# Optimization experiments

Measured on AMD Instinct MI355X. Metric: run time of the kernel, lower is better.

Reference implementation:

```python
import math
import jax, jax.numpy as jnp
import numpy as np

B, S, D, H = 2, 2048, 1024, 16
DH = D // H


def setup_inputs() -> dict:
    key = jax.random.key(0)
    ks = jax.random.split(key, 12)
    s = 1.0 / math.sqrt(D)
    return {
        "x_q": jax.random.normal(ks[0], (B, S, D), jnp.float32),
        "x_k": jax.random.normal(ks[1], (B, S, D), jnp.float32),
        "x_v": jax.random.normal(ks[2], (B, S, D), jnp.float32),
        "mask": jax.random.randint(ks[3], (B, S), 0, 2) > 0,
        "Wq": jax.random.normal(ks[4], (D, D), jnp.float32) * s,
        "bq": jnp.zeros((D,), jnp.float32),
        "Wk": jax.random.normal(ks[5], (D, D), jnp.float32) * s,
        "bk": jnp.zeros((D,), jnp.float32),
        "Wv": jax.random.normal(ks[6], (D, D), jnp.float32) * s,
        "bv": jnp.zeros((D,), jnp.float32),
        "Wo": jax.random.normal(ks[7], (D, D), jnp.float32) * s,
        "bo": jnp.zeros((D,), jnp.float32),
    }


def reference(x_q, x_k, x_v, mask, Wq, bq, Wk, bk, Wv, bv, Wo, bo):
    # nn.Linear: y = x @ W^T + b
    Q = jnp.einsum('bsd,ed->bse', x_q, Wq) + bq
    K = jnp.einsum('bsd,ed->bse', x_k, Wk) + bk
    V = jnp.einsum('bsd,ed->bse', x_v, Wv) + bv
    b, sq, d = Q.shape
    # split(dim_split, 2) + cat(dim=0) == per-head attention on [B,S,H,DH]
    Qh = Q.reshape(b, sq, H, DH)
    Kh = K.reshape(b, -1, H, DH)
    Vh = V.reshape(b, -1, H, DH)
    scores = jnp.einsum('bqhd,bkhd->bhqk', Qh, Kh) / math.sqrt(DH)
    # inf_mask: -1e9 where mask is False, broadcast over heads and queries
    scores = scores + jnp.where(mask[:, None, None, :], 0.0, -1e9)
    A = jax.nn.softmax(scores, axis=-1)  # dropout is identity in eval
    out = jnp.einsum('bhqk,bkhd->bqhd', A, Vh).reshape(b, sq, d)
    return jnp.einsum('bsd,ed->bse', out, Wo) + bo
```

## Files before the change

kernel.cpp:

```cpp
#include <hip/hip_runtime.h>
#include <hip/hip_bf16.h>
#include <stdint.h>

#define BB  2
#define SS  2048
#define DDIM 1024
#define HH  16
#define DH  64

typedef __attribute__((ext_vector_type(8))) short short8;
typedef __attribute__((ext_vector_type(4))) short short4v;
typedef __attribute__((ext_vector_type(4))) float float4v;
typedef __attribute__((ext_vector_type(2))) unsigned int uint2v;

#define AS1 __attribute__((address_space(1)))
#define AS3 __attribute__((address_space(3)))

static __device__ __forceinline__ void gl2lds16(const void* g, void* l) {
  __builtin_amdgcn_global_load_lds((const AS1 unsigned int*)g,
                                   (AS3 unsigned int*)l, 16, 0, 0);
}

static __device__ __forceinline__ float bf2f(short s) {
  union { unsigned u; float f; } c;
  c.u = ((unsigned)(unsigned short)s) << 16;
  return c.f;
}
static __device__ __forceinline__ short f2bf(float f) {
  union { float ff; unsigned u; } c;
  c.ff = f;
  unsigned u = c.u;
  u += 0x7fffu + ((u >> 16) & 1u);
  return (short)(u >> 16);
}

#if __has_builtin(__builtin_amdgcn_exp2f)
static __device__ __forceinline__ float exp2fast(float x) { return __builtin_amdgcn_exp2f(x); }
#else
static __device__ __forceinline__ float exp2fast(float x) { return __expf(x * 0.69314718056f); }
#endif

static __device__ __forceinline__ unsigned packbf(float x, float y) {
  unsigned ax = __float_as_uint(x) + 0x8000u;
  unsigned ay = __float_as_uint(y) + 0x8000u;
#if __has_builtin(__builtin_amdgcn_perm)
  return __builtin_amdgcn_perm(ay, ax, 0x07060302u);
#else
  return (ax >> 16) | (ay & 0xffff0000u);
#endif
}

static __device__ __forceinline__ int detect_f32(const void* p) {
  const float* f = (const float*)p;
  int ok = 1;
#pragma unroll
  for (int i = 0; i < 16; i++) {
    float a = fabsf(f[i]);
    ok &= (a > 1e-10f && a < 1e4f) ? 1 : 0;
  }
  return ok;
}

struct CvtArgs {
  const void* xq; const void* xk; const void* xv;
  const void* wq; const void* wk; const void* wv; const void* wo;
  const void* b0; const void* b1; const void* b2; const void* b3;
  short* dst;
};

__global__ __launch_bounds__(256)
void cvt_kernel(CvtArgs a) {
  const int f32m = detect_f32(a.xq);
  const size_t gtid = (size_t)blockIdx.x * blockDim.x + threadIdx.x;
  const size_t stride = (size_t)gridDim.x * blockDim.x;
  const size_t M4 = (size_t)4 << 20, M1 = (size_t)1 << 20, TOT = (size_t)16 << 20;
  for (size_t i = gtid; i * 4 < TOT; i += stride) {
    const size_t idx = i * 4;
    const void* src;
    size_t off;
    if (idx < 3 * M4) {
      size_t xi = idx / M4;
      off = idx & (M4 - 1);
      src = (xi == 0) ? a.xq : (xi == 1) ? a.xk : a.xv;
    } else {
      size_t wi = (idx - 3 * M4) / M1;
      off = idx & (M1 - 1);
      src = (wi == 0) ? a.wq : (wi == 1) ? a.wk : (wi == 2) ? a.wv : a.wo;
    }
    short4v o;
    if (f32m) {
      float4v v = *(const float4v*)((const float*)src + off);
#pragma unroll
      for (int j = 0; j < 4; j++) o[j] = f2bf(v[j]);
    } else {
      o = *(const short4v*)((const short*)src + off);
    }
    *(short4v*)(a.dst + idx) = o;
  }
  if (gtid < 1024) {
    const void* bs[4] = {a.b0, a.b1, a.b2, a.b3};
#pragma unroll
    for (int j = 0; j < 4; j++) {
      short v = f32m ? f2bf(((const float*)bs[j])[gtid])
                     : ((const short*)bs[j])[gtid];
      a.dst[TOT + (size_t)j * 1024 + gtid] = v;
    }
  }
}

struct GemmArgs {
  const short* x[3];
  const short* w[3];
  const short* b[3];
  short* o[3];
  const void* probe;
  int tmask;
  int detect_out;
};

__global__ __launch_bounds__(256)
void gemm_kernel(GemmArgs a) {
  constexpr int GK = 1024, GN = 1024;
  __shared__ alignas(16) short As[128 * 32];
  __shared__ alignas(16) short Bs[128 * 32];

  const int t = threadIdx.x;
  const int w = t >> 6, l = t & 63, l15 = l & 15, qd = l >> 4;
  const int bn = blockIdx.x, bm = blockIdx.y, mat = blockIdx.z;

  const short* X  = a.x[mat];
  const short* W  = a.w[mat];
  const short* Bi = a.b[mat];
  short* O        = a.o[mat];
  const int transposed = (a.tmask >> mat) & 1;

  const short* Ag = X + (size_t)bm * 128 * GK;
  const short* Bg = W + (size_t)bn * 128 * GK;

  const int L0 = t, L1 = 256 + t;
  const int r0 = L0 >> 2, g0 = (L0 & 3) ^ ((r0 >> 1) & 3);
  const int r1 = L1 >> 2, g1 = (L1 & 3) ^ ((r1 >> 1) & 3);
  const size_t off0 = (size_t)r0 * GK + g0 * 8;
  const size_t off1 = (size_t)r1 * GK + g1 * 8;

  float4v acc[4][4];
#pragma unroll
  for (int i = 0; i < 4; i++)
#pragma unroll
    for (int j = 0; j < 4; j++) acc[i][j] = (float4v){0.f, 0.f, 0.f, 0.f};

  const int wm = (w >> 1) * 64, wn = (w & 1) * 64;

  for (int k0 = 0; k0 < GK; k0 += 32) {
    gl2lds16(Ag + off0 + k0, (char*)As + L0 * 16);
    gl2lds16(Ag + off1 + k0, (char*)As + L1 * 16);
    gl2lds16(Bg + off0 + k0, (char*)Bs + L0 * 16);
    gl2lds16(Bg + off1 + k0, (char*)Bs + L1 * 16);
    __syncthreads();

    short8 af[4], bf[4];
#pragma unroll
    for (int i = 0; i < 4; i++) {
      int m = wm + i * 16 + l15;
      af[i] = *(const short8*)((const char*)As + (m * 4 + (qd ^ ((m >> 1) & 3))) * 16);
      int n = wn + i * 16 + l15;
      bf[i] = *(const short8*)((const char*)Bs + (n * 4 + (qd ^ ((n >> 1) & 3))) * 16);
    }
#pragma unroll
    for (int i = 0; i < 4; i++)
#pragma unroll
      for (int j = 0; j < 4; j++)
        acc[i][j] = __builtin_amdgcn_mfma_f32_16x16x32_bf16(af[i], bf[j], acc[i][j], 0, 0, 0);
    __syncthreads();
  }

  if (!transposed) {
    const int outf32 = a.detect_out ? detect_f32(a.probe) : 0;
    float bj[4];
#pragma unroll
    for (int j = 0; j < 4; j++) bj[j] = bf2f(Bi[bn * 128 + wn + j * 16 + l15]);
#pragma unroll
    for (int i = 0; i < 4; i++) {
      int mgl = bm * 128 + wm + i * 16 + qd * 4;
#pragma unroll
      for (int j = 0; j < 4; j++) {
        int ngl = bn * 128 + wn + j * 16 + l15;
        if (outf32) {
          float* Of = (float*)O;
#pragma unroll
          for (int r = 0; r < 4; r++)
            Of[(size_t)(mgl + r) * GN + ngl] = acc[i][j][r] + bj[j];
        } else {
#pragma unroll
          for (int r = 0; r < 4; r++)
            O[(size_t)(mgl + r) * GN + ngl] = f2bf(acc[i][j][r] + bj[j]);
        }
      }
    }
  } else {
#pragma unroll
    for (int j = 0; j < 4; j++) {
      int ngl = bn * 128 + wn + j * 16 + l15;
      float bb = bf2f(Bi[ngl]);
#pragma unroll
      for (int i = 0; i < 4; i++) {
        int mgl = bm * 128 + wm + i * 16 + qd * 4;
        int bidx = mgl >> 11;
        int s = mgl & (SS - 1);
        short4v v;
#pragma unroll
        for (int r = 0; r < 4; r++) v[r] = f2bf(acc[i][j][r] + bb);
        *(short4v*)(O + (size_t)bidx * DDIM * SS + (size_t)ngl * SS + s) = v;
      }
    }
  }
}

__global__ __launch_bounds__(256)
void flash_kernel(const short* __restrict__ Q, const short* __restrict__ K,
                  const short* __restrict__ Vt, const int* __restrict__ mask,
                  short* __restrict__ Oa) {
  __shared__ alignas(16) short Ks[2][32 * 64];
  __shared__ alignas(16) short Vs[2][64 * 32];
  __shared__ alignas(16) float madd[2][32];
  __shared__ alignas(16) short Ps[4][2][16 * 40];

  const int t = threadIdx.x;
  const int w = t >> 6, l = t & 63, l15 = l & 15, qd = l >> 4;
  const int qt = blockIdx.x, bh = blockIdx.y;
  const int b = bh >> 4, h = bh & 15;
  const int q0 = qt * 128 + w * 32;

  const float SC = 0.125f * 1.44269504f;
  const float MC = 16.0f * 1.44269504f;

  short8 qf[2][2];
#pragma unroll
  for (int g = 0; g < 2; g++) {
    const short* Qb = Q + ((size_t)(b * SS + q0 + 16 * g + l15)) * DDIM + h * 64;
#pragma unroll
    for (int c = 0; c < 2; c++) qf[g][c] = *(const short8*)(Qb + 32 * c + 8 * qd);
  }

  const int kr = t >> 3;
  const short* Kg = K + ((size_t)(b * SS + kr)) * DDIM + h * 64 + (((t & 7) ^ (kr & 7)) * 8);
  const int vr = t >> 2;
  const short* Vg = Vt + (size_t)b * DDIM * SS + (size_t)(h * 64 + vr) * SS
                    + (((t & 3) ^ ((vr >> 1) & 3)) * 8);
  const int* Mg = mask + b * SS;

  const int sw = l15 & 7;
  int kOff[2], vOff[4];
#pragma unroll
  for (int mt = 0; mt < 2; mt++) kOff[mt] = (mt * 16 + l15) * 64 + ((qd ^ sw) * 8);
  const int vchunk = qd ^ ((l15 >> 1) & 3);
#pragma unroll
  for (int mt = 0; mt < 4; mt++) vOff[mt] = (mt * 16 + l15) * 32 + vchunk * 8;

  float4v oacc[2][4];
#pragma unroll
  for (int g = 0; g < 2; g++)
#pragma unroll
    for (int mt = 0; mt < 4; mt++) oacc[g][mt] = (float4v){0.f, 0.f, 0.f, 0.f};
  float lsum[2] = {0.f, 0.f};

  gl2lds16(Kg, (char*)Ks[0] + t * 16);
  gl2lds16(Vg, (char*)Vs[0] + t * 16);
  int mv = 0;
  if (t < 32) {
    mv = Mg[t];
    madd[0][t] = mv ? -MC : -1e9f;
    mv = Mg[32 + t];
  }

  for (int i = 0; i < SS / 32; i++) {
    const int cur = i & 1, nxt = cur ^ 1;
    asm volatile("s_waitcnt vmcnt(0) lgkmcnt(0)\n\ts_barrier" ::: "memory");

    if (i < SS / 32 - 1) {
      gl2lds16(Kg + (size_t)(i + 1) * 32 * DDIM, (char*)Ks[nxt] + t * 16);
      gl2lds16(Vg + (i + 1) * 32, (char*)Vs[nxt] + t * 16);
    }
    if (t < 32) {
      madd[nxt][t] = mv ? -MC : -1e9f;
      int idx = 32 * i + 64 + t;
      if (idx > SS - 1) idx = SS - 1;
      mv = Mg[idx];
    }

    const short* ksb = Ks[cur];
    const short* vsb = Vs[cur];

    float4v sacc[2][2];
#pragma unroll
    for (int g = 0; g < 2; g++)
#pragma unroll
      for (int mt = 0; mt < 2; mt++) sacc[g][mt] = (float4v){0.f, 0.f, 0.f, 0.f};
#pragma unroll
    for (int mt = 0; mt < 2; mt++) {
      short8 kf0 = *(const short8*)(ksb + kOff[mt]);
      short8 kf1 = *(const short8*)(ksb + (kOff[mt] ^ 32));
#pragma unroll
      for (int g = 0; g < 2; g++) {
        sacc[g][mt] = __builtin_amdgcn_mfma_f32_16x16x32_bf16(kf0, qf[g][0], sacc[g][mt], 0, 0, 0);
        sacc[g][mt] = __builtin_amdgcn_mfma_f32_16x16x32_bf16(kf1, qf[g][1], sacc[g][mt], 0, 0, 0);
      }
    }

    float4v ma[2];
#pragma unroll
    for (int mt = 0; mt < 2; mt++)
      ma[mt] = *(const float4v*)(&madd[cur][16 * mt + 4 * qd]);

    short8 vf[4];
#pragma unroll
    for (int mt = 0; mt < 4; mt++) vf[mt] = *(const short8*)(vsb + vOff[mt]);

#pragma unroll
    for (int g = 0; g < 2; g++) {
      float p[2][4];
#pragma unroll
      for (int mt = 0; mt < 2; mt++)
#pragma unroll
        for (int r = 0; r < 4; r++) {
          p[mt][r] = exp2fast(fmaf(sacc[g][mt][r], SC, ma[mt][r]));
          lsum[g] += p[mt][r];
        }
      short* pw = (short*)Ps[w][g] + l15 * 40;
#pragma unroll
      for (int mt = 0; mt < 2; mt++) {
        uint2v pk;
        pk[0] = packbf(p[mt][0], p[mt][1]);
        pk[1] = packbf(p[mt][2], p[mt][3]);
        *(uint2v*)(pw + mt * 16 + qd * 4) = pk;
      }
      asm volatile("s_waitcnt lgkmcnt(0)" ::: "memory");
      short8 pf = *(const short8*)((short*)Ps[w][g] + l15 * 40 + qd * 8);

#pragma unroll
      for (int mt = 0; mt < 4; mt++)
        oacc[g][mt] = __builtin_amdgcn_mfma_f32_16x16x32_bf16(vf[mt], pf, oacc[g][mt], 0, 0, 0);
    }
  }

#pragma unroll
  for (int g = 0; g < 2; g++) {
    lsum[g] += __shfl_xor(lsum[g], 16);
    lsum[g] += __shfl_xor(lsum[g], 32);
    const float inv = 1.f / lsum[g];
    short* Og = Oa + ((size_t)(b * SS + q0 + 16 * g + l15)) * DDIM + h * 64;
#pragma unroll
    for (int mt = 0; mt < 4; mt++) {
      short4v v;
#pragma unroll
      for (int r = 0; r < 4; r++) v[r] = f2bf(oacc[g][mt][r] * inv);
      *(short4v*)(Og + mt * 16 + qd * 4) = v;
    }
  }
}

extern "C" void kernel_launch(void* const* d_in, const int* in_sizes, int n_in,
                              void* d_out, int out_size, void* d_ws, size_t ws_size,
                              hipStream_t stream) {
  (void)in_sizes; (void)n_in; (void)out_size; (void)ws_size;
  const int* mask = (const int*)d_in[3];

  char* ws = (char*)d_ws;
  short* wsBF = (short*)ws;
  const size_t M1 = (size_t)1 << 20;
  short* Qb = (short*)(ws + (size_t)34 * M1);
  short* Kb = (short*)(ws + (size_t)42 * M1);
  short* Vt = (short*)(ws + (size_t)50 * M1);
  short* At = (short*)(ws + (size_t)58 * M1);

  CvtArgs c;
  c.xq = d_in[0]; c.xk = d_in[1]; c.xv = d_in[2];
  c.wq = d_in[4]; c.wk = d_in[6]; c.wv = d_in[8]; c.wo = d_in[10];
  c.b0 = d_in[5]; c.b1 = d_in[7]; c.b2 = d_in[9]; c.b3 = d_in[11];
  c.dst = wsBF;
  hipLaunchKernelGGL(cvt_kernel, dim3(4096), dim3(256), 0, stream, c);

  GemmArgs a1;
  a1.x[0] = wsBF;            a1.x[1] = wsBF + 4 * M1;  a1.x[2] = wsBF + 8 * M1;
  a1.w[0] = wsBF + 12 * M1;  a1.w[1] = wsBF + 13 * M1; a1.w[2] = wsBF + 14 * M1;
  a1.b[0] = wsBF + 16 * M1;  a1.b[1] = wsBF + 16 * M1 + 1024;
  a1.b[2] = wsBF + 16 * M1 + 2048;
  a1.o[0] = Qb; a1.o[1] = Kb; a1.o[2] = Vt;
  a1.probe = d_in[0];
  a1.tmask = 4;
  a1.detect_out = 0;
  hipLaunchKernelGGL(gemm_kernel, dim3(8, 32, 3), dim3(256), 0, stream, a1);

  hipLaunchKernelGGL(flash_kernel, dim3(16, 32), dim3(256), 0, stream,
                     Qb, Kb, Vt, mask, At);

  GemmArgs a2;
  a2.x[0] = At;             a2.w[0] = wsBF + 15 * M1;
  a2.b[0] = wsBF + 16 * M1 + 3072;
  a2.o[0] = (short*)d_out;
  a2.x[1] = a2.x[2] = At; a2.w[1] = a2.w[2] = a2.w[0];
  a2.b[1] = a2.b[2] = a2.b[0]; a2.o[1] = a2.o[2] = a2.o[0];
  a2.probe = d_in[0];
  a2.tmask = 0;
  a2.detect_out = 1;
  hipLaunchKernelGGL(gemm_kernel, dim3(8, 32, 1), dim3(256), 0, stream, a2);
}
```

Measured before the change: 258.7 us.

## Split flash attention over the key dimension and add a combine kernel

The flash kernel grid gains a key-split dimension (two halves when workspace permits). Each split writes fp32 partial outputs and row sums, and a new combine kernel adds them, normalizes and writes bf16. The row sum is now computed by an extra MFMA against a ones vector instead of scalar adds and shuffles. This doubles the flash grid from 512 blocks to improve occupancy on the many CUs, at the cost of extra fp32 partial traffic (about 32MB written and read) and one more launch.

```diff
diff --git a/kernel.cpp b/kernel.cpp
--- a/kernel.cpp
+++ b/kernel.cpp
@@ -219,7 +219,8 @@
 __global__ __launch_bounds__(256)
 void flash_kernel(const short* __restrict__ Q, const short* __restrict__ K,
                   const short* __restrict__ Vt, const int* __restrict__ mask,
-                  short* __restrict__ Oa) {
+                  short* __restrict__ At, float* __restrict__ Op,
+                  float* __restrict__ Lw, int nsplit) {
   __shared__ alignas(16) short Ks[2][32 * 64];
   __shared__ alignas(16) short Vs[2][64 * 32];
   __shared__ alignas(16) float madd[2][32];
@@ -227,9 +228,11 @@
 
   const int t = threadIdx.x;
   const int w = t >> 6, l = t & 63, l15 = l & 15, qd = l >> 4;
-  const int qt = blockIdx.x, bh = blockIdx.y;
+  const int qt = blockIdx.x, bh = blockIdx.y, split = blockIdx.z;
   const int b = bh >> 4, h = bh & 15;
   const int q0 = qt * 128 + w * 32;
+  const int kspan = SS / nsplit;
+  const int kbase = split * kspan;
 
   const float SC = 0.125f * 1.44269504f;
   const float MC = 16.0f * 1.44269504f;
@@ -242,12 +245,17 @@
     for (int c = 0; c < 2; c++) qf[g][c] = *(const short8*)(Qb + 32 * c + 8 * qd);
   }
 
+  const short onebf = (short)0x3F80;
+  const short ov = (l15 == 0) ? onebf : (short)0;
+  const short8 onesf = {ov, ov, ov, ov, ov, ov, ov, ov};
+
   const int kr = t >> 3;
-  const short* Kg = K + ((size_t)(b * SS + kr)) * DDIM + h * 64 + (((t & 7) ^ (kr & 7)) * 8);
+  const short* Kg = K + ((size_t)(b * SS + kbase + kr)) * DDIM + h * 64
+                    + (((t & 7) ^ (kr & 7)) * 8);
   const int vr = t >> 2;
   const short* Vg = Vt + (size_t)b * DDIM * SS + (size_t)(h * 64 + vr) * SS
-                    + (((t & 3) ^ ((vr >> 1) & 3)) * 8);
-  const int* Mg = mask + b * SS;
+                    + kbase + (((t & 3) ^ ((vr >> 1) & 3)) * 8);
+  const int* Mg = mask + b * SS + kbase;
 
   const int sw = l15 & 7;
   int kOff[2], vOff[4];
@@ -258,11 +266,13 @@
   for (int mt = 0; mt < 4; mt++) vOff[mt] = (mt * 16 + l15) * 32 + vchunk * 8;
 
   float4v oacc[2][4];
-#pragma unroll
-  for (int g = 0; g < 2; g++)
+  float4v oaccl[2];
+#pragma unroll
+  for (int g = 0; g < 2; g++) {
+    oaccl[g] = (float4v){0.f, 0.f, 0.f, 0.f};
 #pragma unroll
     for (int mt = 0; mt < 4; mt++) oacc[g][mt] = (float4v){0.f, 0.f, 0.f, 0.f};
-  float lsum[2] = {0.f, 0.f};
+  }
 
   gl2lds16(Kg, (char*)Ks[0] + t * 16);
   gl2lds16(Vg, (char*)Vs[0] + t * 16);
@@ -273,18 +283,19 @@
     mv = Mg[32 + t];
   }
 
-  for (int i = 0; i < SS / 32; i++) {
+  const int niter = kspan / 32;
+  for (int i = 0; i < niter; i++) {
     const int cur = i & 1, nxt = cur ^ 1;
     asm volatile("s_waitcnt vmcnt(0) lgkmcnt(0)\n\ts_barrier" ::: "memory");
 
-    if (i < SS / 32 - 1) {
+    if (i < niter - 1) {
       gl2lds16(Kg + (size_t)(i + 1) * 32 * DDIM, (char*)Ks[nxt] + t * 16);
       gl2lds16(Vg + (i + 1) * 32, (char*)Vs[nxt] + t * 16);
     }
     if (t < 32) {
       madd[nxt][t] = mv ? -MC : -1e9f;
       int idx = 32 * i + 64 + t;
-      if (idx > SS - 1) idx = SS - 1;
+      if (idx > kspan - 1) idx = kspan - 1;
       mv = Mg[idx];
     }
 
@@ -322,10 +333,8 @@
 #pragma unroll
       for (int mt = 0; mt < 2; mt++)
 #pragma unroll
-        for (int r = 0; r < 4; r++) {
+        for (int r = 0; r < 4; r++)
           p[mt][r] = exp2fast(fmaf(sacc[g][mt][r], SC, ma[mt][r]));
-          lsum[g] += p[mt][r];
-        }
       short* pw = (short*)Ps[w][g] + l15 * 40;
 #pragma unroll
       for (int mt = 0; mt < 2; mt++) {
@@ -340,29 +349,61 @@
 #pragma unroll
       for (int mt = 0; mt < 4; mt++)
         oacc[g][mt] = __builtin_amdgcn_mfma_f32_16x16x32_bf16(vf[mt], pf, oacc[g][mt], 0, 0, 0);
-    }
-  }
-
-#pragma unroll
-  for (int g = 0; g < 2; g++) {
-    lsum[g] += __shfl_xor(lsum[g], 16);
-    lsum[g] += __shfl_xor(lsum[g], 32);
-    const float inv = 1.f / lsum[g];
-    short* Og = Oa + ((size_t)(b * SS + q0 + 16 * g + l15)) * DDIM + h * 64;
-#pragma unroll
-    for (int mt = 0; mt < 4; mt++) {
-      short4v v;
-#pragma unroll
-      for (int r = 0; r < 4; r++) v[r] = f2bf(oacc[g][mt][r] * inv);
-      *(short4v*)(Og + mt * 16 + qd * 4) = v;
-    }
-  }
+      oaccl[g] = __builtin_amdgcn_mfma_f32_16x16x32_bf16(onesf, pf, oaccl[g], 0, 0, 0);
+    }
+  }
+
+  if (nsplit == 2) {
+    float* OpS = Op + (size_t)split * ((size_t)4 << 20);
+#pragma unroll
+    for (int g = 0; g < 2; g++) {
+      const int q = q0 + 16 * g + l15;
+      float* base = OpS + ((size_t)(b * SS + q)) * DDIM + h * 64;
+#pragma unroll
+      for (int mt = 0; mt < 4; mt++)
+        *(float4v*)(base + mt * 16 + qd * 4) = oacc[g][mt];
+      if (qd == 0)
+        Lw[split * (BB * HH * SS) + (b * HH + h) * SS + q] = oaccl[g][0];
+    }
+  } else {
+#pragma unroll
+    for (int g = 0; g < 2; g++) {
+      const float lg = __shfl(oaccl[g][0], l15);
+      const float inv = 1.f / lg;
+      short* Og = At + ((size_t)(b * SS + q0 + 16 * g + l15)) * DDIM + h * 64;
+#pragma unroll
+      for (int mt = 0; mt < 4; mt++) {
+        short4v v;
+#pragma unroll
+        for (int r = 0; r < 4; r++) v[r] = f2bf(oacc[g][mt][r] * inv);
+        *(short4v*)(Og + mt * 16 + qd * 4) = v;
+      }
+    }
+  }
+}
+
+__global__ __launch_bounds__(256)
+void combine_kernel(const float* __restrict__ Op, const float* __restrict__ Lw,
+                    short* __restrict__ At) {
+  const int tid = blockIdx.x * 256 + threadIdx.x;
+  const size_t e4 = (size_t)tid * 4;
+  const int row = (int)(e4 >> 10);
+  const int col = (int)(e4 & 1023);
+  const int b = row >> 11, q = row & (SS - 1), h = col >> 6;
+  float4v o0 = *(const float4v*)(Op + e4);
+  float4v o1 = *(const float4v*)(Op + ((size_t)4 << 20) + e4);
+  const int li = (b * HH + h) * SS + q;
+  const float inv = 1.f / (Lw[li] + Lw[BB * HH * SS + li]);
+  short4v v;
+#pragma unroll
+  for (int r = 0; r < 4; r++) v[r] = f2bf((o0[r] + o1[r]) * inv);
+  *(short4v*)(At + e4) = v;
 }
 
 extern "C" void kernel_launch(void* const* d_in, const int* in_sizes, int n_in,
                               void* d_out, int out_size, void* d_ws, size_t ws_size,
                               hipStream_t stream) {
-  (void)in_sizes; (void)n_in; (void)out_size; (void)ws_size;
+  (void)in_sizes; (void)n_in; (void)out_size;
   const int* mask = (const int*)d_in[3];
 
   char* ws = (char*)d_ws;
@@ -372,6 +413,10 @@
   short* Kb = (short*)(ws + (size_t)42 * M1);
   short* Vt = (short*)(ws + (size_t)50 * M1);
   short* At = (short*)(ws + (size_t)58 * M1);
+  float* Op = (float*)(ws + (size_t)66 * M1);
+  float* Lw = (float*)(ws + (size_t)98 * M1);
+
+  const int nsplit = (ws_size >= (size_t)99 * M1) ? 2 : 1;
 
   CvtArgs c;
   c.xq = d_in[0]; c.xk = d_in[1]; c.xv = d_in[2];
@@ -391,8 +436,12 @@
   a1.detect_out = 0;
   hipLaunchKernelGGL(gemm_kernel, dim3(8, 32, 3), dim3(256), 0, stream, a1);
 
-  hipLaunchKernelGGL(flash_kernel, dim3(16, 32), dim3(256), 0, stream,
-                     Qb, Kb, Vt, mask, At);
+  hipLaunchKernelGGL(flash_kernel, dim3(16, 32, nsplit), dim3(256), 0, stream,
+                     Qb, Kb, Vt, mask, At, Op, Lw, nsplit);
+
+  if (nsplit == 2)
+    hipLaunchKernelGGL(combine_kernel, dim3(4096), dim3(256), 0, stream,
+                       Op, Lw, At);
 
   GemmArgs a2;
   a2.x[0] = At;             a2.w[0] = wsBF + 15 * M1;
```

New measurement: 272.5 us. 1.05x slower.

## Make flash attention warp-private with per-warp KV staging, MFMA row sums, precomputed mask

Applied to the files above, without the earlier changes.

Restructures the flash kernel so each 64-lane wave loads its own K/V tiles into private LDS double buffers, which removes block-wide barriers. Blocks shrink to 128 threads and the grid is reordered. P is packed straight into MFMA operand registers instead of round-tripping through LDS. Row sums are computed with an extra MFMA against a ones vector, and the mask additive term is precomputed once in the convert kernel into a float workspace. The cost is duplicated K/V loads per wave, more global traffic, and an extra MFMA per step.

```diff
diff --git a/kernel.cpp b/kernel.cpp
--- a/kernel.cpp
+++ b/kernel.cpp
@@ -11,7 +11,6 @@
 typedef __attribute__((ext_vector_type(8))) short short8;
 typedef __attribute__((ext_vector_type(4))) short short4v;
 typedef __attribute__((ext_vector_type(4))) float float4v;
-typedef __attribute__((ext_vector_type(2))) unsigned int uint2v;
 
 #define AS1 __attribute__((address_space(1)))
 #define AS3 __attribute__((address_space(3)))
@@ -65,7 +64,9 @@
   const void* xq; const void* xk; const void* xv;
   const void* wq; const void* wk; const void* wv; const void* wo;
   const void* b0; const void* b1; const void* b2; const void* b3;
+  const int* mask;
   short* dst;
+  float* mw;
 };
 
 __global__ __launch_bounds__(256)
@@ -106,6 +107,8 @@
       a.dst[TOT + (size_t)j * 1024 + gtid] = v;
     }
   }
+  if (gtid < BB * SS)
+    a.mw[gtid] = a.mask[gtid] ? -23.083120654223414f : -1e9f;
 }
 
 struct GemmArgs {
@@ -216,23 +219,20 @@
   }
 }
 
-__global__ __launch_bounds__(256)
+__global__ __launch_bounds__(128)
 void flash_kernel(const short* __restrict__ Q, const short* __restrict__ K,
-                  const short* __restrict__ Vt, const int* __restrict__ mask,
-                  short* __restrict__ Oa) {
-  __shared__ alignas(16) short Ks[2][32 * 64];
-  __shared__ alignas(16) short Vs[2][64 * 32];
-  __shared__ alignas(16) float madd[2][32];
-  __shared__ alignas(16) short Ps[4][2][16 * 40];
+                  const short* __restrict__ Vt, const float* __restrict__ Mw,
+                  short* __restrict__ At) {
+  __shared__ alignas(16) short Kbuf[2][2][2048];
+  __shared__ alignas(16) short Vbuf[2][2][2048];
 
   const int t = threadIdx.x;
   const int w = t >> 6, l = t & 63, l15 = l & 15, qd = l >> 4;
-  const int qt = blockIdx.x, bh = blockIdx.y;
+  const int bh = blockIdx.x, qt = blockIdx.y;
   const int b = bh >> 4, h = bh & 15;
-  const int q0 = qt * 128 + w * 32;
+  const int q0 = qt * 64 + w * 32;
 
   const float SC = 0.125f * 1.44269504f;
-  const float MC = 16.0f * 1.44269504f;
 
   short8 qf[2][2];
 #pragma unroll
@@ -242,54 +242,63 @@
     for (int c = 0; c < 2; c++) qf[g][c] = *(const short8*)(Qb + 32 * c + 8 * qd);
   }
 
-  const int kr = t >> 3;
-  const short* Kg = K + ((size_t)(b * SS + kr)) * DDIM + h * 64 + (((t & 7) ^ (kr & 7)) * 8);
-  const int vr = t >> 2;
-  const short* Vg = Vt + (size_t)b * DDIM * SS + (size_t)(h * 64 + vr) * SS
-                    + (((t & 3) ^ ((vr >> 1) & 3)) * 8);
-  const int* Mg = mask + b * SS;
-
-  const int sw = l15 & 7;
-  int kOff[2], vOff[4];
-#pragma unroll
-  for (int mt = 0; mt < 2; mt++) kOff[mt] = (mt * 16 + l15) * 64 + ((qd ^ sw) * 8);
-  const int vchunk = qd ^ ((l15 >> 1) & 3);
-#pragma unroll
-  for (int mt = 0; mt < 4; mt++) vOff[mt] = (mt * 16 + l15) * 32 + vchunk * 8;
-
-  float4v oacc[2][4];
-#pragma unroll
-  for (int g = 0; g < 2; g++)
+  const short ov = (l15 == 0) ? (short)0x3F80 : (short)0;
+  const short8 onesf = {ov, ov, ov, ov, ov, ov, ov, ov};
+
+  const short* Kg = K + ((size_t)(b * SS + (l >> 3))) * DDIM + h * 64
+                    + ((l & 7) ^ ((l >> 3) & 7)) * 8;
+  const short* Vg = Vt + (size_t)b * DDIM * SS + (size_t)(h * 64 + (l >> 2)) * SS
+                    + ((l & 3) ^ ((l >> 3) & 3)) * 8;
+  const float* MwB = Mw + b * SS;
+
+  char* Kw = (char*)Kbuf[w];
+  char* Vw = (char*)Vbuf[w];
+
+  float4v oacc[2][4], oaccl[2];
+#pragma unroll
+  for (int g = 0; g < 2; g++) {
+    oaccl[g] = (float4v){0.f, 0.f, 0.f, 0.f};
 #pragma unroll
     for (int mt = 0; mt < 4; mt++) oacc[g][mt] = (float4v){0.f, 0.f, 0.f, 0.f};
-  float lsum[2] = {0.f, 0.f};
-
-  gl2lds16(Kg, (char*)Ks[0] + t * 16);
-  gl2lds16(Vg, (char*)Vs[0] + t * 16);
-  int mv = 0;
-  if (t < 32) {
-    mv = Mg[t];
-    madd[0][t] = mv ? -MC : -1e9f;
-    mv = Mg[32 + t];
-  }
-
-  for (int i = 0; i < SS / 32; i++) {
-    const int cur = i & 1, nxt = cur ^ 1;
-    asm volatile("s_waitcnt vmcnt(0) lgkmcnt(0)\n\ts_barrier" ::: "memory");
-
-    if (i < SS / 32 - 1) {
-      gl2lds16(Kg + (size_t)(i + 1) * 32 * DDIM, (char*)Ks[nxt] + t * 16);
-      gl2lds16(Vg + (i + 1) * 32, (char*)Vs[nxt] + t * 16);
-    }
-    if (t < 32) {
-      madd[nxt][t] = mv ? -MC : -1e9f;
-      int idx = 32 * i + 64 + t;
-      if (idx > SS - 1) idx = SS - 1;
-      mv = Mg[idx];
-    }
-
-    const short* ksb = Ks[cur];
-    const short* vsb = Vs[cur];
+  }
+
+  const int sv2 = 2 * ((l15 >> 1) & 3);
+  const int kswz = l15 & 7;
+
+  float4v maC[2], maN[2];
+
+  {
+#pragma unroll
+    for (int j = 0; j < 4; j++)
+      gl2lds16(Kg + (size_t)(j * 8) * DDIM, Kw + j * 1024 + (l << 4));
+#pragma unroll
+    for (int j = 0; j < 4; j++)
+      gl2lds16(Vg + (size_t)(j * 16) * SS, Vw + j * 1024 + (l << 4));
+#pragma unroll
+    for (int mt = 0; mt < 2; mt++)
+      maC[mt] = *(const float4v*)(MwB + mt * 16 + 4 * qd);
+  }
+
+  auto body = [&](int i, int bb) {
+    asm volatile("s_waitcnt vmcnt(0)" ::: "memory");
+
+    if (i < 63) {
+      const int nb = bb ^ 1;
+      const size_t koff = (size_t)((i + 1) * 32) * DDIM;
+#pragma unroll
+      for (int j = 0; j < 4; j++)
+        gl2lds16(Kg + koff + (size_t)(j * 8) * DDIM, Kw + nb * 4096 + j * 1024 + (l << 4));
+      const int voff = (i + 1) * 32;
+#pragma unroll
+      for (int j = 0; j < 4; j++)
+        gl2lds16(Vg + voff + (size_t)(j * 16) * SS, Vw + nb * 4096 + j * 1024 + (l << 4));
+#pragma unroll
+      for (int mt = 0; mt < 2; mt++)
+        maN[mt] = *(const float4v*)(MwB + (i + 1) * 32 + mt * 16 + 4 * qd);
+    }
+
+    const short* ksb = (const short*)(Kw + bb * 4096);
+    const short* vsb = (const short*)(Vw + bb * 4096);
 
     float4v sacc[2][2];
 #pragma unroll
@@ -297,58 +306,58 @@
 #pragma unroll
       for (int mt = 0; mt < 2; mt++) sacc[g][mt] = (float4v){0.f, 0.f, 0.f, 0.f};
 #pragma unroll
-    for (int mt = 0; mt < 2; mt++) {
-      short8 kf0 = *(const short8*)(ksb + kOff[mt]);
-      short8 kf1 = *(const short8*)(ksb + (kOff[mt] ^ 32));
-#pragma unroll
-      for (int g = 0; g < 2; g++) {
-        sacc[g][mt] = __builtin_amdgcn_mfma_f32_16x16x32_bf16(kf0, qf[g][0], sacc[g][mt], 0, 0, 0);
-        sacc[g][mt] = __builtin_amdgcn_mfma_f32_16x16x32_bf16(kf1, qf[g][1], sacc[g][mt], 0, 0, 0);
+    for (int c = 0; c < 2; c++) {
+#pragma unroll
+      for (int mt = 0; mt < 2; mt++) {
+        short8 kf = *(const short8*)(ksb + (mt * 16 + l15) * 64 + (((c * 4 + qd) ^ kswz) * 8));
+#pragma unroll
+        for (int g = 0; g < 2; g++)
+          sacc[g][mt] = __builtin_amdgcn_mfma_f32_16x16x32_bf16(kf, qf[g][c], sacc[g][mt], 0, 0, 0);
       }
     }
 
-    float4v ma[2];
-#pragma unroll
-    for (int mt = 0; mt < 2; mt++)
-      ma[mt] = *(const float4v*)(&madd[cur][16 * mt + 4 * qd]);
-
-    short8 vf[4];
-#pragma unroll
-    for (int mt = 0; mt < 4; mt++) vf[mt] = *(const short8*)(vsb + vOff[mt]);
+    union { short4v h[2]; short8 v8; } vf[4];
+#pragma unroll
+    for (int mt = 0; mt < 4; mt++) {
+      const short* vr = vsb + (mt * 16 + l15) * 32;
+      vf[mt].h[0] = *(const short4v*)(vr + ((qd ^ sv2) * 4));
+      vf[mt].h[1] = *(const short4v*)(vr + (((4 + qd) ^ sv2) * 4));
+    }
 
 #pragma unroll
     for (int g = 0; g < 2; g++) {
-      float p[2][4];
-#pragma unroll
-      for (int mt = 0; mt < 2; mt++)
-#pragma unroll
-        for (int r = 0; r < 4; r++) {
-          p[mt][r] = exp2fast(fmaf(sacc[g][mt][r], SC, ma[mt][r]));
-          lsum[g] += p[mt][r];
-        }
-      short* pw = (short*)Ps[w][g] + l15 * 40;
-#pragma unroll
-      for (int mt = 0; mt < 2; mt++) {
-        uint2v pk;
-        pk[0] = packbf(p[mt][0], p[mt][1]);
-        pk[1] = packbf(p[mt][2], p[mt][3]);
-        *(uint2v*)(pw + mt * 16 + qd * 4) = pk;
+      float p0[4], p1[4];
+#pragma unroll
+      for (int r = 0; r < 4; r++) {
+        p0[r] = exp2fast(fmaf(sacc[g][0][r], SC, maC[0][r]));
+        p1[r] = exp2fast(fmaf(sacc[g][1][r], SC, maC[1][r]));
       }
-      asm volatile("s_waitcnt lgkmcnt(0)" ::: "memory");
-      short8 pf = *(const short8*)((short*)Ps[w][g] + l15 * 40 + qd * 8);
+      union { unsigned u[4]; short8 v8; } pk;
+      pk.u[0] = packbf(p0[0], p0[1]);
+      pk.u[1] = packbf(p0[2], p0[3]);
+      pk.u[2] = packbf(p1[0], p1[1]);
+      pk.u[3] = packbf(p1[2], p1[3]);
 
 #pragma unroll
       for (int mt = 0; mt < 4; mt++)
-        oacc[g][mt] = __builtin_amdgcn_mfma_f32_16x16x32_bf16(vf[mt], pf, oacc[g][mt], 0, 0, 0);
-    }
+        oacc[g][mt] = __builtin_amdgcn_mfma_f32_16x16x32_bf16(vf[mt].v8, pk.v8, oacc[g][mt], 0, 0, 0);
+      oaccl[g] = __builtin_amdgcn_mfma_f32_16x16x32_bf16(onesf, pk.v8, oaccl[g], 0, 0, 0);
+    }
+
+    maC[0] = maN[0];
+    maC[1] = maN[1];
+  };
+
+  for (int i = 0; i < 64; i += 2) {
+    body(i, 0);
+    body(i + 1, 1);
   }
 
 #pragma unroll
   for (int g = 0; g < 2; g++) {
-    lsum[g] += __shfl_xor(lsum[g], 16);
-    lsum[g] += __shfl_xor(lsum[g], 32);
-    const float inv = 1.f / lsum[g];
-    short* Og = Oa + ((size_t)(b * SS + q0 + 16 * g + l15)) * DDIM + h * 64;
+    const float lg = __shfl(oaccl[g][0], l15);
+    const float inv = 1.f / lg;
+    short* Og = At + ((size_t)(b * SS + q0 + 16 * g + l15)) * DDIM + h * 64;
 #pragma unroll
     for (int mt = 0; mt < 4; mt++) {
       short4v v;
@@ -372,12 +381,13 @@
   short* Kb = (short*)(ws + (size_t)42 * M1);
   short* Vt = (short*)(ws + (size_t)50 * M1);
   short* At = (short*)(ws + (size_t)58 * M1);
+  float* Mw = (float*)(ws + (size_t)66 * M1);
 
   CvtArgs c;
   c.xq = d_in[0]; c.xk = d_in[1]; c.xv = d_in[2];
   c.wq = d_in[4]; c.wk = d_in[6]; c.wv = d_in[8]; c.wo = d_in[10];
   c.b0 = d_in[5]; c.b1 = d_in[7]; c.b2 = d_in[9]; c.b3 = d_in[11];
-  c.dst = wsBF;
+  c.mask = mask; c.dst = wsBF; c.mw = Mw;
   hipLaunchKernelGGL(cvt_kernel, dim3(4096), dim3(256), 0, stream, c);
 
   GemmArgs a1;
@@ -391,8 +401,8 @@
   a1.detect_out = 0;
   hipLaunchKernelGGL(gemm_kernel, dim3(8, 32, 3), dim3(256), 0, stream, a1);
 
-  hipLaunchKernelGGL(flash_kernel, dim3(16, 32), dim3(256), 0, stream,
-                     Qb, Kb, Vt, mask, At);
+  hipLaunchKernelGGL(flash_kernel, dim3(32, 32), dim3(128), 0, stream,
+                     Qb, Kb, Vt, Mw, At);
 
   GemmArgs a2;
   a2.x[0] = At;             a2.w[0] = wsBF + 15 * M1;
```

After: 263.4 us. No clear change (+1.8%).
